# Kernel optimization log

Hardware: AMD Instinct MI355X
Metric: run time of the kernel (lower is better)

Reference implementation:

```python
import jax, jax.numpy as jnp
import numpy as np

N = 50000
E = 800000
F = 128
HID = 128
C = 40
GAMMA = 0.1
EPS = 0.1


def gcn(x, theta, src, dst, n):
    # GCNConv (bias=False) with added self-loops and symmetric normalization.
    xw = x @ theta  # [N, d]
    ones = jnp.ones(src.shape[0], dtype=x.dtype)
    deg = jax.ops.segment_sum(ones, dst, num_segments=n) + 1.0  # in-degree incl. self loop
    dinv = jax.lax.rsqrt(deg)
    norm = dinv[src] * dinv[dst]            # [E]
    msg = xw[src] * norm[:, None]           # [E, d]  (dominant memory traffic)
    agg = jax.ops.segment_sum(msg, dst, num_segments=n)
    return agg + xw * (dinv * dinv)[:, None]  # self-loop contribution


def antisym_conv(x, W, bias, theta, src, dst, n):
    # PyG AntiSymmetricConv, num_iters=1, act=tanh, eps=0.1, gamma=0.1
    M = W - W.T - GAMMA * jnp.eye(W.shape[0], dtype=x.dtype)
    h = gcn(x, theta, src, dst, n)
    h = x @ M.T + h + bias
    return x + EPS * jnp.tanh(h)


def setup_inputs() -> dict:
    key = jax.random.key(0)
    ks = jax.random.split(key, 12)
    s = 0.05
    return {
        "x": jax.random.normal(ks[0], (N, F), dtype=jnp.float32),
        "edge_index": jax.random.randint(ks[1], (2, E), 0, N, dtype=jnp.int64)
        if jax.config.jax_enable_x64 else jax.random.randint(ks[1], (2, E), 0, N, dtype=jnp.int32),
        # AntiSymmetricConv 1 (num_features channels)
        "W1": jax.random.normal(ks[2], (F, F), dtype=jnp.float32) * s,
        "b1": jnp.zeros((F,), dtype=jnp.float32),
        "T1": jax.random.normal(ks[3], (F, F), dtype=jnp.float32) * s,
        # AntiSymmetricConv 2 (nhid channels)
        "W2": jax.random.normal(ks[4], (HID, HID), dtype=jnp.float32) * s,
        "b2": jnp.zeros((HID,), dtype=jnp.float32),
        "T2": jax.random.normal(ks[5], (HID, HID), dtype=jnp.float32) * s,
        # Linear layers (torch convention: weight [out, in])
        "lw1": jax.random.normal(ks[6], (HID, F), dtype=jnp.float32) * s,
        "lb1": jnp.zeros((HID,), dtype=jnp.float32),
        "lw2": jax.random.normal(ks[7], (C, HID), dtype=jnp.float32) * s,
        "lb2": jnp.zeros((C,), dtype=jnp.float32),
    }


def reference(x, edge_index, W1, b1, T1, W2, b2, T2, lw1, lb1, lw2, lb2):
    src, dst = edge_index[0], edge_index[1]
    n = x.shape[0]
    # eval mode: dropout is identity
    h = antisym_conv(x, W1, b1, T1, src, dst, n)
    h = jax.nn.relu(h)
    h = h @ lw1.T + lb1
    h = jax.nn.relu(h)
    h = antisym_conv(h, W2, b2, T2, src, dst, n)
    h = jax.nn.relu(h)
    x1 = h
    logits = h @ lw2.T + lb2
    result = jax.nn.log_softmax(logits, axis=-1)
    return (result, x1)
```

## Files before the change

### kernel.cpp

```cpp
#include <hip/hip_runtime.h>
#include <hip/hip_bf16.h>
#include <math.h>

#define GAMMA_ 0.1f
#define EPS_ 0.1f
constexpr int BLK = 256;

typedef __attribute__((ext_vector_type(8))) short short8;
typedef __attribute__((ext_vector_type(4))) float f32x4;
typedef __attribute__((ext_vector_type(2))) float f32x2v;
typedef unsigned char u8;

__device__ inline float bflo(uint u) { union { uint i; float f; } v; v.i = u << 16; return v.f; }
__device__ inline float bfhi(uint u) { union { uint i; float f; } v; v.i = u & 0xffff0000u; return v.f; }
__device__ inline ushort f2bf(float f) {
  union { float f; uint i; } v; v.f = f;
  uint i = v.i;
  return (ushort)((i + 0x7fffu + ((i >> 16) & 1u)) >> 16);
}

#if __has_builtin(__builtin_amdgcn_cvt_pk_f32_fp8) && __has_builtin(__builtin_amdgcn_cvt_pk_fp8_f32)
#define HW_FP8 1
#endif

__device__ inline f32x2v fp8x2_dec(uint raw) {
#ifdef HW_FP8
  return __builtin_amdgcn_cvt_pk_f32_fp8(raw, false);
#else
  f32x2v r;
#pragma unroll
  for (int i = 0; i < 2; ++i) {
    uint b = (raw >> (8 * i)) & 0xffu;
    uint em = b & 0x7fu;
    union { uint u; float f; } o;
    o.u = ((b & 0x80u) << 24) | (0x3C000000u + (em << 20));
    r[i] = (em >= 8u) ? o.f : 0.f;
  }
  return r;
#endif
}

__device__ inline uint fp8enc1(float x) {
  union { float f; uint u; } v; v.f = x;
  uint s = (v.u >> 24) & 0x80u;
  uint a = v.u & 0x7fffffffu;
  if (a >= 0x43E00000u) return s | 0x7Eu;
  uint r = a + 0x7FFFFu + ((a >> 20) & 1u);
  if (r < 0x3D800000u) return s;
  return s | (((r - 0x3C000000u) >> 20) & 0x7fu);
}

template<bool HI>
__device__ inline uint fp8x2_enc(float f0, float f1, uint old) {
#ifdef HW_FP8
  return __builtin_amdgcn_cvt_pk_fp8_f32(f0, f1, old, HI);
#else
  uint p = fp8enc1(f0) | (fp8enc1(f1) << 8);
  return HI ? ((old & 0x0000ffffu) | (p << 16)) : ((old & 0xffff0000u) | p);
#endif
}

__global__ void k_init(int* cnt, int n) {
  int i = blockIdx.x * BLK + threadIdx.x;
  if (i < n) cnt[i] = 0;
}

__global__ void k_count(const int* __restrict__ dst, int* cnt,
                        int* __restrict__ rank, int e) {
  int i = blockIdx.x * BLK + threadIdx.x;
  if (i < e) rank[i] = atomicAdd(&cnt[dst[i]], 1);
}

__global__ void k_scan1(const int* __restrict__ cnt, int* __restrict__ rowp,
                        int* __restrict__ bsum, int n) {
  __shared__ int s[BLK];
  int t = threadIdx.x;
  int i = blockIdx.x * BLK + t;
  int v = (i < n) ? cnt[i] : 0;
  s[t] = v; __syncthreads();
  for (int off = 1; off < BLK; off <<= 1) {
    int u = (t >= off) ? s[t - off] : 0;
    __syncthreads();
    s[t] += u;
    __syncthreads();
  }
  if (i < n) rowp[i] = s[t] - v;
  if (t == BLK - 1) bsum[blockIdx.x] = s[t];
}

__global__ void k_scan2(const int* __restrict__ bsum, int* __restrict__ boff, int nb) {
  __shared__ int s[BLK];
  int t = threadIdx.x;
  int v = (t < nb) ? bsum[t] : 0;
  s[t] = v; __syncthreads();
  for (int off = 1; off < BLK; off <<= 1) {
    int u = (t >= off) ? s[t - off] : 0;
    __syncthreads();
    s[t] += u;
    __syncthreads();
  }
  if (t < nb) boff[t] = s[t] - v;
}

__global__ void k_scan3(const int* __restrict__ boff, int* __restrict__ rowp,
                        const int* __restrict__ cnt, float* __restrict__ dinv,
                        int n, int e) {
  int i = blockIdx.x * BLK + threadIdx.x;
  if (i < n) {
    rowp[i] += boff[blockIdx.x];
    dinv[i] = rsqrtf((float)cnt[i] + 1.0f);
    if (i == 0) rowp[n] = e;
  }
}

__global__ void k_fill(const int* __restrict__ src, const int* __restrict__ dst,
                       const int* __restrict__ rowp, const int* __restrict__ rank,
                       int* __restrict__ csrc, int e) {
  int i = blockIdx.x * BLK + threadIdx.x;
  if (i < e) {
    int d = dst[i];
    csrc[rowp[d] + rank[i]] = src[i];
  }
}

__global__ void k_pack(const float* __restrict__ W1, const float* __restrict__ T1,
                       const float* __restrict__ W2, const float* __restrict__ T2,
                       const float* __restrict__ lw1, const float* __restrict__ lw2,
                       ushort* __restrict__ Bpk1, ushort* __restrict__ Bpk2,
                       ushort* __restrict__ Bpkl, ushort* __restrict__ Bpk2l) {
  int idx = blockIdx.x * BLK + threadIdx.x;
  if (idx < 65536) {
    int which = idx >> 15;
    int e = idx & 32767;
    int k = e >> 8, c = e & 255;
    const float* W = which ? W2 : W1;
    const float* T = which ? T2 : T1;
    float v;
    if (c < 128) {
      v = T[k * 128 + c];
    } else {
      int cc = c - 128;
      v = W[cc * 128 + k] - W[k * 128 + cc] - ((cc == k) ? GAMMA_ : 0.f);
    }
    int kt = k >> 5, q = (k >> 3) & 3, j = k & 7;
    ushort* B = which ? Bpk2 : Bpk1;
    B[(((kt * 4 + q) * 256 + c) << 3) + j] = f2bf(v);
  } else if (idx < 81920) {
    int e = idx - 65536;
    int k = e >> 7, c = e & 127;
    float v = lw1[c * 128 + k];
    int kt = k >> 5, q = (k >> 3) & 3, j = k & 7;
    Bpkl[(((kt * 4 + q) * 128 + c) << 3) + j] = f2bf(v);
  } else {
    int e = idx - 81920;
    if (e < 6144) {
      int k = e / 48, c = e - k * 48;
      float v = (c < 40) ? lw2[c * 128 + k] : 0.f;
      int kt = k >> 5, q = (k >> 3) & 3, j = k & 7;
      Bpk2l[(((kt * 4 + q) * 48 + c) << 3) + j] = f2bf(v);
    }
  }
}

template<int NC, bool SPLIT, bool FP32A>
__global__ __launch_bounds__(256) void k_mgemm(
    const void* __restrict__ Av, int nrows,
    const ushort* __restrict__ Bpk, const float* __restrict__ bias,
    const float* __restrict__ dinv,
    ushort* __restrict__ O0, ushort* __restrict__ O1, u8* __restrict__ Oq) {
  constexpr int NCW = NC / 4;
  constexpr int NT = NCW / 16;
  __shared__ ushort Cs[32 * NC];
  const int t = threadIdx.x;
  const int w = t >> 6, l = t & 63;
  const int lr = l & 15, lq = l >> 4;
  const int r0 = blockIdx.x * 32;
  const int ar0 = min(r0 + lr, nrows - 1);
  const int ar1 = min(r0 + 16 + lr, nrows - 1);
  f32x4 acc[2][NT];
#pragma unroll
  for (int rf = 0; rf < 2; ++rf)
#pragma unroll
    for (int n = 0; n < NT; ++n) acc[rf][n] = f32x4{0.f, 0.f, 0.f, 0.f};
#pragma unroll
  for (int kt = 0; kt < 4; ++kt) {
    short8 af0, af1;
    if (FP32A) {
      const float* Ap0 = (const float*)Av + (size_t)ar0 * 128 + lq * 8 + kt * 32;
      const float* Ap1 = (const float*)Av + (size_t)ar1 * 128 + lq * 8 + kt * 32;
      float4 a0 = *(const float4*)(Ap0), a0b = *(const float4*)(Ap0 + 4);
      float4 a1 = *(const float4*)(Ap1), a1b = *(const float4*)(Ap1 + 4);
      af0[0] = (short)f2bf(a0.x); af0[1] = (short)f2bf(a0.y);
      af0[2] = (short)f2bf(a0.z); af0[3] = (short)f2bf(a0.w);
      af0[4] = (short)f2bf(a0b.x); af0[5] = (short)f2bf(a0b.y);
      af0[6] = (short)f2bf(a0b.z); af0[7] = (short)f2bf(a0b.w);
      af1[0] = (short)f2bf(a1.x); af1[1] = (short)f2bf(a1.y);
      af1[2] = (short)f2bf(a1.z); af1[3] = (short)f2bf(a1.w);
      af1[4] = (short)f2bf(a1b.x); af1[5] = (short)f2bf(a1b.y);
      af1[6] = (short)f2bf(a1b.z); af1[7] = (short)f2bf(a1b.w);
    } else {
      af0 = *(const short8*)((const ushort*)Av + (size_t)ar0 * 128 + lq * 8 + kt * 32);
      af1 = *(const short8*)((const ushort*)Av + (size_t)ar1 * 128 + lq * 8 + kt * 32);
    }
    const ushort* bbase = Bpk + ((size_t)((kt * 4 + lq) * NC) + w * NCW + lr) * 8;
#pragma unroll
    for (int n = 0; n < NT; ++n) {
      short8 bf = *(const short8*)(bbase + n * 16 * 8);
      acc[0][n] = __builtin_amdgcn_mfma_f32_16x16x32_bf16(af0, bf, acc[0][n], 0, 0, 0);
      acc[1][n] = __builtin_amdgcn_mfma_f32_16x16x32_bf16(af1, bf, acc[1][n], 0, 0, 0);
    }
  }
#pragma unroll
  for (int rf = 0; rf < 2; ++rf)
#pragma unroll
    for (int n = 0; n < NT; ++n)
#pragma unroll
      for (int r = 0; r < 4; ++r) {
        int row = rf * 16 + lq * 4 + r;
        int col = w * NCW + n * 16 + lr;
        float v = acc[rf][n][r];
        if (!SPLIT) v = fmaxf(v + bias[col], 0.f);
        int pcol = col ^ (((row >> 2) & 3) << 3);
        Cs[row * NC + pcol] = f2bf(v);
      }
  __syncthreads();
  if (SPLIT) {
#pragma unroll
    for (int it = 0; it < 2; ++it) {
      int idx = it * 256 + t;
      int row = idx >> 4, c8 = idx & 15;
      if (r0 + row < nrows) {
        int pc = (16 + (c8 ^ ((row >> 2) & 3))) * 8;
        uint4 v = *(const uint4*)(Cs + row * 256 + pc);
        *(uint4*)(O1 + (size_t)(r0 + row) * 128 + c8 * 8) = v;
      }
    }
#pragma unroll
    for (int it = 0; it < 2; ++it) {
      int idx = it * 256 + t;
      int row = idx >> 4, c8 = idx & 15;
      if (r0 + row < nrows) {
        float di = dinv[r0 + row];
        int pc = (c8 ^ ((row >> 2) & 3)) * 8;
        const uint* p = (const uint*)(Cs + row * 256 + pc);
        uint u0 = p[0], u1 = p[1], u2 = p[2], u3 = p[3];
        uint lo = fp8x2_enc<false>(bflo(u0) * di, bfhi(u0) * di, 0u);
        lo = fp8x2_enc<true>(bflo(u1) * di, bfhi(u1) * di, lo);
        uint hi = fp8x2_enc<false>(bflo(u2) * di, bfhi(u2) * di, 0u);
        hi = fp8x2_enc<true>(bflo(u3) * di, bfhi(u3) * di, hi);
        uint2 ov = { lo, hi };
        *(uint2*)(Oq + (size_t)(r0 + row) * 128 + c8 * 8) = ov;
      }
    }
  } else {
#pragma unroll
    for (int it = 0; it < 2; ++it) {
      int idx = it * 256 + t;
      int row = idx >> 4, c8 = idx & 15;
      if (r0 + row < nrows) {
        int pc = (c8 ^ ((row >> 2) & 3)) * 8;
        uint4 v = *(const uint4*)(Cs + row * 128 + pc);
        *(uint4*)(O0 + (size_t)(r0 + row) * 128 + c8 * 8) = v;
      }
    }
  }
}

template<bool XIN_BF, bool OUT_BF>
__global__ __launch_bounds__(256) void k_aggc(
    const u8* __restrict__ xq, const ushort* __restrict__ xmb,
    const float* __restrict__ xinf, const ushort* __restrict__ xinb,
    const float* __restrict__ dinv,
    const int* __restrict__ rowp, const int* __restrict__ csrc,
    const float* __restrict__ bias,
    float* __restrict__ outf, ushort* __restrict__ outb, int n) {
  int node = blockIdx.x * 4 + (threadIdx.x >> 6);
  if (node >= n) return;
  int l = threadIdx.x & 63;
  uint su = *(const ushort*)(xq + (size_t)node * 128 + 2 * l);
  f32x2v sf = fp8x2_dec(su);
  float a0 = sf[0], a1 = sf[1];
  int e0 = rowp[node], e1 = rowp[node + 1];
  int e = e0;
  for (; e + 7 < e1; e += 8) {
    int s[8];
#pragma unroll
    for (int u = 0; u < 8; ++u) s[u] = csrc[e + u];
    uint g[8];
#pragma unroll
    for (int u = 0; u < 8; ++u)
      g[u] = *(const ushort*)(xq + (size_t)s[u] * 128 + 2 * l);
#pragma unroll
    for (int u = 0; u < 8; ++u) {
      f32x2v f = fp8x2_dec(g[u]);
      a0 += f[0]; a1 += f[1];
    }
  }
  if (e + 3 < e1) {
    int s[4];
#pragma unroll
    for (int u = 0; u < 4; ++u) s[u] = csrc[e + u];
    uint g[4];
#pragma unroll
    for (int u = 0; u < 4; ++u)
      g[u] = *(const ushort*)(xq + (size_t)s[u] * 128 + 2 * l);
#pragma unroll
    for (int u = 0; u < 4; ++u) {
      f32x2v f = fp8x2_dec(g[u]);
      a0 += f[0]; a1 += f[1];
    }
    e += 4;
  }
  for (; e < e1; ++e) {
    uint g0 = *(const ushort*)(xq + (size_t)csrc[e] * 128 + 2 * l);
    f32x2v f = fp8x2_dec(g0);
    a0 += f[0]; a1 += f[1];
  }
  float di = dinv[node];
  uint mu = *(const uint*)(xmb + (size_t)node * 128 + 2 * l);
  float h0 = a0 * di + bflo(mu) + bias[2 * l];
  float h1 = a1 * di + bfhi(mu) + bias[2 * l + 1];
  float x0, x1v;
  if (XIN_BF) {
    uint xu = *(const uint*)(xinb + (size_t)node * 128 + 2 * l);
    x0 = bflo(xu); x1v = bfhi(xu);
  } else {
    float2 xv = *(const float2*)(xinf + (size_t)node * 128 + 2 * l);
    x0 = xv.x; x1v = xv.y;
  }
  float o0 = fmaxf(x0 + EPS_ * tanhf(h0), 0.f);
  float o1 = fmaxf(x1v + EPS_ * tanhf(h1), 0.f);
  if (OUT_BF) {
    ushort2 o = { f2bf(o0), f2bf(o1) };
    *(ushort2*)(outb + (size_t)node * 128 + 2 * l) = o;
  } else {
    float2 o = { o0, o1 };
    *(float2*)(outf + (size_t)node * 128 + 2 * l) = o;
  }
}

__global__ __launch_bounds__(256) void k_logits2(
    const float* __restrict__ X, const ushort* __restrict__ Bpk,
    const float* __restrict__ lb2, float* __restrict__ out, int n) {
  __shared__ float Ls[64 * 49];
  __shared__ float bl[48];
  const int t = threadIdx.x;
  if (t < 48) bl[t] = (t < 40) ? lb2[t] : 0.f;
  const int w = t >> 6, l = t & 63;
  const int lr = l & 15, lq = l >> 4;
  const int r0 = blockIdx.x * 64;
  const int ar = min(r0 + w * 16 + lr, n - 1);
  const float* Ap = X + (size_t)ar * 128 + lq * 8;
  f32x4 acc[3];
#pragma unroll
  for (int nn = 0; nn < 3; ++nn) acc[nn] = f32x4{0.f, 0.f, 0.f, 0.f};
#pragma unroll
  for (int kt = 0; kt < 4; ++kt) {
    float4 xa = *(const float4*)(Ap + kt * 32);
    float4 xc = *(const float4*)(Ap + kt * 32 + 4);
    short8 af;
    af[0] = (short)f2bf(xa.x); af[1] = (short)f2bf(xa.y);
    af[2] = (short)f2bf(xa.z); af[3] = (short)f2bf(xa.w);
    af[4] = (short)f2bf(xc.x); af[5] = (short)f2bf(xc.y);
    af[6] = (short)f2bf(xc.z); af[7] = (short)f2bf(xc.w);
    const ushort* bbase = Bpk + ((size_t)((kt * 4 + lq) * 48) + lr) * 8;
#pragma unroll
    for (int nn = 0; nn < 3; ++nn) {
      short8 bf = *(const short8*)(bbase + nn * 16 * 8);
      acc[nn] = __builtin_amdgcn_mfma_f32_16x16x32_bf16(af, bf, acc[nn], 0, 0, 0);
    }
  }
  __syncthreads();
#pragma unroll
  for (int nn = 0; nn < 3; ++nn)
#pragma unroll
    for (int r = 0; r < 4; ++r) {
      int row = w * 16 + lq * 4 + r;
      int col = nn * 16 + lr;
      Ls[row * 49 + col] = acc[nn][r] + bl[col];
    }
  __syncthreads();
  int row = t >> 2, q = t & 3;
  if (r0 + row >= n) return;
  const float* Lr = Ls + row * 49 + q * 10;
  float m = -1e30f;
#pragma unroll
  for (int c = 0; c < 10; ++c) m = fmaxf(m, Lr[c]);
  m = fmaxf(m, __shfl_xor(m, 1));
  m = fmaxf(m, __shfl_xor(m, 2));
  float s = 0.f;
#pragma unroll
  for (int c = 0; c < 10; ++c) s += expf(Lr[c] - m);
  s += __shfl_xor(s, 1);
  s += __shfl_xor(s, 2);
  float lse = m + logf(s);
  float* Or = out + (size_t)(r0 + row) * 40 + q * 10;
#pragma unroll
  for (int c = 0; c < 10; ++c) Or[c] = Lr[c] - lse;
}

extern "C" void kernel_launch(void* const* d_in, const int* in_sizes, int n_in,
                              void* d_out, int out_size, void* d_ws, size_t ws_size,
                              hipStream_t stream) {
  const float* x   = (const float*)d_in[0];
  const int*   ei  = (const int*)d_in[1];
  const float* W1  = (const float*)d_in[2];
  const float* b1  = (const float*)d_in[3];
  const float* T1  = (const float*)d_in[4];
  const float* W2  = (const float*)d_in[5];
  const float* b2  = (const float*)d_in[6];
  const float* T2  = (const float*)d_in[7];
  const float* lw1 = (const float*)d_in[8];
  const float* lb1 = (const float*)d_in[9];
  const float* lw2 = (const float*)d_in[10];
  const float* lb2 = (const float*)d_in[11];
  const int N = in_sizes[0] / 128;
  const int E = in_sizes[1] / 2;
  const int* src = ei;
  const int* dst = ei + E;

  float* ws = (float*)d_ws;
  size_t o = 0;
  float* dinv = ws;             o += N;
  int* cnt = (int*)(ws + o);    o += N;
  int* rowp = (int*)(ws + o);   o += (size_t)(N + 4);
  int* csrc = (int*)(ws + o);   o += E;
  int* rank = (int*)(ws + o);   o += E;
  int* bsum = (int*)(ws + o);   o += 256;
  int* boff = (int*)(ws + o);   o += 256;
  o = (o + 3) & ~(size_t)3;
  ushort* us = (ushort*)(ws + o);
  size_t uo = 0;
  ushort* Bpk1 = us + uo;       uo += 32768;
  ushort* Bpk2 = us + uo;       uo += 32768;
  ushort* Bpkl = us + uo;       uo += 16384;
  ushort* Bpk2l = us + uo;      uo += 6144;
  ushort* xmb  = us + uo;       uo += (size_t)N * 128;
  ushort* h1b  = us + uo;       uo += (size_t)N * 128;
  ushort* h2b  = us + uo;       uo += (size_t)N * 128;
  u8* xq = (u8*)(us + uo);

  float* outp = (float*)d_out;
  float* x1 = outp + (size_t)N * 40;

  int nb_n = (N + BLK - 1) / BLK;
  int nb_e = (E + BLK - 1) / BLK;
  int nb_r = (N + 31) / 32;

  k_init<<<nb_n, BLK, 0, stream>>>(cnt, N);
  k_count<<<nb_e, BLK, 0, stream>>>(dst, cnt, rank, E);
  k_scan1<<<nb_n, BLK, 0, stream>>>(cnt, rowp, bsum, N);
  k_scan2<<<1, BLK, 0, stream>>>(bsum, boff, nb_n);
  k_scan3<<<nb_n, BLK, 0, stream>>>(boff, rowp, cnt, dinv, N, E);
  k_fill<<<nb_e, BLK, 0, stream>>>(src, dst, rowp, rank, csrc, E);
  k_pack<<<344, BLK, 0, stream>>>(W1, T1, W2, T2, lw1, lw2, Bpk1, Bpk2, Bpkl, Bpk2l);

  k_mgemm<256, true, true><<<nb_r, 256, 0, stream>>>(
      x, N, Bpk1, nullptr, dinv, nullptr, xmb, xq);
  k_aggc<false, true><<<(N + 3) / 4, 256, 0, stream>>>(
      xq, xmb, x, nullptr, dinv, rowp, csrc, b1, nullptr, h1b, N);
  k_mgemm<128, false, false><<<nb_r, 256, 0, stream>>>(
      h1b, N, Bpkl, lb1, nullptr, h2b, nullptr, nullptr);
  k_mgemm<256, true, false><<<nb_r, 256, 0, stream>>>(
      h2b, N, Bpk2, nullptr, dinv, nullptr, xmb, xq);
  k_aggc<true, false><<<(N + 3) / 4, 256, 0, stream>>>(
      xq, xmb, nullptr, h2b, dinv, rowp, csrc, b2, x1, nullptr, N);
  k_logits2<<<(N + 63) / 64, 256, 0, stream>>>(x1, Bpk2l, lb2, outp, N);
}
```

Measured before the change: 192.8 us.

## Fuse first aggregation with lin1 GEMM and retile GEMM to 64-row LDS blocks

Adds a new kernel that performs the layer-1 neighbour aggregation for 32 nodes, stages the bf16 results in shared memory, and applies the lin1 MFMA GEMM with bias and ReLU in the same kernel. This removes the h1 intermediate buffer round-trip and one launch. The split GEMM now processes 64 rows per block with the A tile staged in swizzled LDS, so each B fragment is reused across four row tiles. The count-buffer init kernel is replaced by hipMemsetAsync. The fused kernel uses 512-thread blocks with serialized per-warp aggregation, which may reduce latency hiding on the gather.

```diff
diff --git a/kernel.cpp b/kernel.cpp
--- a/kernel.cpp
+++ b/kernel.cpp
@@ -58,11 +58,6 @@
   uint p = fp8enc1(f0) | (fp8enc1(f1) << 8);
   return HI ? ((old & 0x0000ffffu) | (p << 16)) : ((old & 0xffff0000u) | p);
 #endif
-}
-
-__global__ void k_init(int* cnt, int n) {
-  int i = blockIdx.x * BLK + threadIdx.x;
-  if (i < n) cnt[i] = 0;
 }
 
 __global__ void k_count(const int* __restrict__ dst, int* cnt,
@@ -162,118 +157,198 @@
   }
 }
 
-template<int NC, bool SPLIT, bool FP32A>
+template<bool FP32A>
 __global__ __launch_bounds__(256) void k_mgemm(
     const void* __restrict__ Av, int nrows,
-    const ushort* __restrict__ Bpk, const float* __restrict__ bias,
-    const float* __restrict__ dinv,
-    ushort* __restrict__ O0, ushort* __restrict__ O1, u8* __restrict__ Oq) {
-  constexpr int NCW = NC / 4;
-  constexpr int NT = NCW / 16;
-  __shared__ ushort Cs[32 * NC];
+    const ushort* __restrict__ Bpk, const float* __restrict__ dinv,
+    ushort* __restrict__ O1, u8* __restrict__ Oq) {
+  __shared__ ushort S[64 * 256];
+  const int t = threadIdx.x;
+  const int w = t >> 6, l = t & 63;
+  const int lr = l & 15, lq = l >> 4;
+  const int r0 = blockIdx.x * 64;
+#pragma unroll
+  for (int it = 0; it < 4; ++it) {
+    int chunk = it * 256 + t;
+    int row = chunk >> 4, c16 = chunk & 15;
+    int gr = min(r0 + row, nrows - 1);
+    ushort* p = S + row * 128 + (c16 ^ (row & 7)) * 8;
+    if (FP32A) {
+      const float* A = (const float*)Av + (size_t)gr * 128 + c16 * 8;
+      float4 v0 = *(const float4*)(A);
+      float4 v1 = *(const float4*)(A + 4);
+      ushort4 o0 = {f2bf(v0.x), f2bf(v0.y), f2bf(v0.z), f2bf(v0.w)};
+      ushort4 o1 = {f2bf(v1.x), f2bf(v1.y), f2bf(v1.z), f2bf(v1.w)};
+      *(ushort4*)(p) = o0;
+      *(ushort4*)(p + 4) = o1;
+    } else {
+      const ushort* A = (const ushort*)Av + (size_t)gr * 128 + c16 * 8;
+      *(uint4*)p = *(const uint4*)A;
+    }
+  }
+  __syncthreads();
+  f32x4 acc[4][4];
+#pragma unroll
+  for (int rt = 0; rt < 4; ++rt)
+#pragma unroll
+    for (int n = 0; n < 4; ++n) acc[rt][n] = f32x4{0.f, 0.f, 0.f, 0.f};
+#pragma unroll
+  for (int kt = 0; kt < 4; ++kt) {
+    short8 af[4];
+#pragma unroll
+    for (int rt = 0; rt < 4; ++rt) {
+      int row = rt * 16 + lr;
+      af[rt] = *(const short8*)(S + row * 128 + ((kt * 4 + lq) ^ (row & 7)) * 8);
+    }
+    const ushort* bbase = Bpk + ((size_t)((kt * 4 + lq) * 256) + w * 64 + lr) * 8;
+#pragma unroll
+    for (int n = 0; n < 4; ++n) {
+      short8 bf = *(const short8*)(bbase + n * 16 * 8);
+#pragma unroll
+      for (int rt = 0; rt < 4; ++rt)
+        acc[rt][n] = __builtin_amdgcn_mfma_f32_16x16x32_bf16(af[rt], bf, acc[rt][n], 0, 0, 0);
+    }
+  }
+  __syncthreads();
+#pragma unroll
+  for (int rt = 0; rt < 4; ++rt)
+#pragma unroll
+    for (int n = 0; n < 4; ++n)
+#pragma unroll
+      for (int r = 0; r < 4; ++r) {
+        int row = rt * 16 + lq * 4 + r;
+        int col = w * 64 + n * 16 + lr;
+        int pcol = col ^ (((row >> 2) & 3) << 3);
+        S[row * 256 + pcol] = f2bf(acc[rt][n][r]);
+      }
+  __syncthreads();
+#pragma unroll
+  for (int it = 0; it < 4; ++it) {
+    int idx = it * 256 + t;
+    int row = idx >> 4, c8 = idx & 15;
+    if (r0 + row < nrows) {
+      int pc = (16 + (c8 ^ ((row >> 2) & 3))) * 8;
+      uint4 v = *(const uint4*)(S + row * 256 + pc);
+      *(uint4*)(O1 + (size_t)(r0 + row) * 128 + c8 * 8) = v;
+    }
+  }
+#pragma unroll
+  for (int it = 0; it < 4; ++it) {
+    int idx = it * 256 + t;
+    int row = idx >> 4, c8 = idx & 15;
+    if (r0 + row < nrows) {
+      float di = dinv[r0 + row];
+      int pc = (c8 ^ ((row >> 2) & 3)) * 8;
+      const uint* p = (const uint*)(S + row * 256 + pc);
+      uint u0 = p[0], u1 = p[1], u2 = p[2], u3 = p[3];
+      uint lo = fp8x2_enc<false>(bflo(u0) * di, bfhi(u0) * di, 0u);
+      lo = fp8x2_enc<true>(bflo(u1) * di, bfhi(u1) * di, lo);
+      uint hi = fp8x2_enc<false>(bflo(u2) * di, bfhi(u2) * di, 0u);
+      hi = fp8x2_enc<true>(bflo(u3) * di, bfhi(u3) * di, hi);
+      uint2 ov = { lo, hi };
+      *(uint2*)(Oq + (size_t)(r0 + row) * 128 + c8 * 8) = ov;
+    }
+  }
+}
+
+__global__ __launch_bounds__(512) void k_aggl(
+    const u8* __restrict__ xq, const ushort* __restrict__ xmb,
+    const float* __restrict__ xinf, const float* __restrict__ dinv,
+    const int* __restrict__ rowp, const int* __restrict__ csrc,
+    const float* __restrict__ bias, const ushort* __restrict__ Bpkl,
+    const float* __restrict__ lb1, ushort* __restrict__ h2b, int n) {
+  __shared__ ushort Hs[32 * 128];
   const int t = threadIdx.x;
   const int w = t >> 6, l = t & 63;
   const int lr = l & 15, lq = l >> 4;
   const int r0 = blockIdx.x * 32;
-  const int ar0 = min(r0 + lr, nrows - 1);
-  const int ar1 = min(r0 + 16 + lr, nrows - 1);
-  f32x4 acc[2][NT];
-#pragma unroll
-  for (int rf = 0; rf < 2; ++rf)
-#pragma unroll
-    for (int n = 0; n < NT; ++n) acc[rf][n] = f32x4{0.f, 0.f, 0.f, 0.f};
+#pragma unroll
+  for (int i = 0; i < 4; ++i) {
+    int lrow = w * 4 + i;
+    int node = r0 + lrow;
+    float o0 = 0.f, o1 = 0.f;
+    if (node < n) {
+      uint su = *(const ushort*)(xq + (size_t)node * 128 + 2 * l);
+      f32x2v sf = fp8x2_dec(su);
+      float a0 = sf[0], a1 = sf[1];
+      int e0 = rowp[node], e1 = rowp[node + 1];
+      int e = e0;
+      for (; e + 7 < e1; e += 8) {
+        int s[8];
+#pragma unroll
+        for (int u = 0; u < 8; ++u) s[u] = csrc[e + u];
+        uint g[8];
+#pragma unroll
+        for (int u = 0; u < 8; ++u)
+          g[u] = *(const ushort*)(xq + (size_t)s[u] * 128 + 2 * l);
+#pragma unroll
+        for (int u = 0; u < 8; ++u) {
+          f32x2v f = fp8x2_dec(g[u]);
+          a0 += f[0]; a1 += f[1];
+        }
+      }
+      if (e + 3 < e1) {
+        int s[4];
+#pragma unroll
+        for (int u = 0; u < 4; ++u) s[u] = csrc[e + u];
+        uint g[4];
+#pragma unroll
+        for (int u = 0; u < 4; ++u)
+          g[u] = *(const ushort*)(xq + (size_t)s[u] * 128 + 2 * l);
+#pragma unroll
+        for (int u = 0; u < 4; ++u) {
+          f32x2v f = fp8x2_dec(g[u]);
+          a0 += f[0]; a1 += f[1];
+        }
+        e += 4;
+      }
+      for (; e < e1; ++e) {
+        uint g0 = *(const ushort*)(xq + (size_t)csrc[e] * 128 + 2 * l);
+        f32x2v f = fp8x2_dec(g0);
+        a0 += f[0]; a1 += f[1];
+      }
+      float di = dinv[node];
+      uint mu = *(const uint*)(xmb + (size_t)node * 128 + 2 * l);
+      float h0 = a0 * di + bflo(mu) + bias[2 * l];
+      float h1 = a1 * di + bfhi(mu) + bias[2 * l + 1];
+      float2 xv = *(const float2*)(xinf + (size_t)node * 128 + 2 * l);
+      o0 = fmaxf(xv.x + EPS_ * tanhf(h0), 0.f);
+      o1 = fmaxf(xv.y + EPS_ * tanhf(h1), 0.f);
+    }
+    ushort2 o = { f2bf(o0), f2bf(o1) };
+    *(ushort2*)(Hs + lrow * 128 + ((l >> 2) ^ (lrow & 7)) * 8 + (l & 3) * 2) = o;
+  }
+  __syncthreads();
+  f32x4 acc[2];
+  acc[0] = f32x4{0.f, 0.f, 0.f, 0.f};
+  acc[1] = f32x4{0.f, 0.f, 0.f, 0.f};
 #pragma unroll
   for (int kt = 0; kt < 4; ++kt) {
-    short8 af0, af1;
-    if (FP32A) {
-      const float* Ap0 = (const float*)Av + (size_t)ar0 * 128 + lq * 8 + kt * 32;
-      const float* Ap1 = (const float*)Av + (size_t)ar1 * 128 + lq * 8 + kt * 32;
-      float4 a0 = *(const float4*)(Ap0), a0b = *(const float4*)(Ap0 + 4);
-      float4 a1 = *(const float4*)(Ap1), a1b = *(const float4*)(Ap1 + 4);
-      af0[0] = (short)f2bf(a0.x); af0[1] = (short)f2bf(a0.y);
-      af0[2] = (short)f2bf(a0.z); af0[3] = (short)f2bf(a0.w);
-      af0[4] = (short)f2bf(a0b.x); af0[5] = (short)f2bf(a0b.y);
-      af0[6] = (short)f2bf(a0b.z); af0[7] = (short)f2bf(a0b.w);
-      af1[0] = (short)f2bf(a1.x); af1[1] = (short)f2bf(a1.y);
-      af1[2] = (short)f2bf(a1.z); af1[3] = (short)f2bf(a1.w);
-      af1[4] = (short)f2bf(a1b.x); af1[5] = (short)f2bf(a1b.y);
-      af1[6] = (short)f2bf(a1b.z); af1[7] = (short)f2bf(a1b.w);
-    } else {
-      af0 = *(const short8*)((const ushort*)Av + (size_t)ar0 * 128 + lq * 8 + kt * 32);
-      af1 = *(const short8*)((const ushort*)Av + (size_t)ar1 * 128 + lq * 8 + kt * 32);
-    }
-    const ushort* bbase = Bpk + ((size_t)((kt * 4 + lq) * NC) + w * NCW + lr) * 8;
-#pragma unroll
-    for (int n = 0; n < NT; ++n) {
-      short8 bf = *(const short8*)(bbase + n * 16 * 8);
-      acc[0][n] = __builtin_amdgcn_mfma_f32_16x16x32_bf16(af0, bf, acc[0][n], 0, 0, 0);
-      acc[1][n] = __builtin_amdgcn_mfma_f32_16x16x32_bf16(af1, bf, acc[1][n], 0, 0, 0);
-    }
-  }
-#pragma unroll
-  for (int rf = 0; rf < 2; ++rf)
-#pragma unroll
-    for (int n = 0; n < NT; ++n)
-#pragma unroll
-      for (int r = 0; r < 4; ++r) {
-        int row = rf * 16 + lq * 4 + r;
-        int col = w * NCW + n * 16 + lr;
-        float v = acc[rf][n][r];
-        if (!SPLIT) v = fmaxf(v + bias[col], 0.f);
-        int pcol = col ^ (((row >> 2) & 3) << 3);
-        Cs[row * NC + pcol] = f2bf(v);
-      }
-  __syncthreads();
-  if (SPLIT) {
-#pragma unroll
-    for (int it = 0; it < 2; ++it) {
-      int idx = it * 256 + t;
-      int row = idx >> 4, c8 = idx & 15;
-      if (r0 + row < nrows) {
-        int pc = (16 + (c8 ^ ((row >> 2) & 3))) * 8;
-        uint4 v = *(const uint4*)(Cs + row * 256 + pc);
-        *(uint4*)(O1 + (size_t)(r0 + row) * 128 + c8 * 8) = v;
-      }
-    }
-#pragma unroll
-    for (int it = 0; it < 2; ++it) {
-      int idx = it * 256 + t;
-      int row = idx >> 4, c8 = idx & 15;
-      if (r0 + row < nrows) {
-        float di = dinv[r0 + row];
-        int pc = (c8 ^ ((row >> 2) & 3)) * 8;
-        const uint* p = (const uint*)(Cs + row * 256 + pc);
-        uint u0 = p[0], u1 = p[1], u2 = p[2], u3 = p[3];
-        uint lo = fp8x2_enc<false>(bflo(u0) * di, bfhi(u0) * di, 0u);
-        lo = fp8x2_enc<true>(bflo(u1) * di, bfhi(u1) * di, lo);
-        uint hi = fp8x2_enc<false>(bflo(u2) * di, bfhi(u2) * di, 0u);
-        hi = fp8x2_enc<true>(bflo(u3) * di, bfhi(u3) * di, hi);
-        uint2 ov = { lo, hi };
-        *(uint2*)(Oq + (size_t)(r0 + row) * 128 + c8 * 8) = ov;
-      }
-    }
-  } else {
-#pragma unroll
-    for (int it = 0; it < 2; ++it) {
-      int idx = it * 256 + t;
-      int row = idx >> 4, c8 = idx & 15;
-      if (r0 + row < nrows) {
-        int pc = (c8 ^ ((row >> 2) & 3)) * 8;
-        uint4 v = *(const uint4*)(Cs + row * 128 + pc);
-        *(uint4*)(O0 + (size_t)(r0 + row) * 128 + c8 * 8) = v;
-      }
-    }
-  }
-}
-
-template<bool XIN_BF, bool OUT_BF>
+    short8 bf = *(const short8*)(Bpkl + ((size_t)((kt * 4 + lq) * 128) + w * 16 + lr) * 8);
+#pragma unroll
+    for (int rt = 0; rt < 2; ++rt) {
+      int row = rt * 16 + lr;
+      short8 af = *(const short8*)(Hs + row * 128 + ((kt * 4 + lq) ^ (row & 7)) * 8);
+      acc[rt] = __builtin_amdgcn_mfma_f32_16x16x32_bf16(af, bf, acc[rt], 0, 0, 0);
+    }
+  }
+  int col = w * 16 + lr;
+  float bv = lb1[col];
+#pragma unroll
+  for (int rt = 0; rt < 2; ++rt)
+#pragma unroll
+    for (int r = 0; r < 4; ++r) {
+      int row = rt * 16 + lq * 4 + r;
+      if (r0 + row < n)
+        h2b[(size_t)(r0 + row) * 128 + col] = f2bf(fmaxf(acc[rt][r] + bv, 0.f));
+    }
+}
+
 __global__ __launch_bounds__(256) void k_aggc(
     const u8* __restrict__ xq, const ushort* __restrict__ xmb,
-    const float* __restrict__ xinf, const ushort* __restrict__ xinb,
-    const float* __restrict__ dinv,
+    const ushort* __restrict__ xinb, const float* __restrict__ dinv,
     const int* __restrict__ rowp, const int* __restrict__ csrc,
-    const float* __restrict__ bias,
-    float* __restrict__ outf, ushort* __restrict__ outb, int n) {
+    const float* __restrict__ bias, float* __restrict__ outf, int n) {
   int node = blockIdx.x * 4 + (threadIdx.x >> 6);
   if (node >= n) return;
   int l = threadIdx.x & 63;
@@ -320,23 +395,11 @@
   uint mu = *(const uint*)(xmb + (size_t)node * 128 + 2 * l);
   float h0 = a0 * di + bflo(mu) + bias[2 * l];
   float h1 = a1 * di + bfhi(mu) + bias[2 * l + 1];
-  float x0, x1v;
-  if (XIN_BF) {
-    uint xu = *(const uint*)(xinb + (size_t)node * 128 + 2 * l);
-    x0 = bflo(xu); x1v = bfhi(xu);
-  } else {
-    float2 xv = *(const float2*)(xinf + (size_t)node * 128 + 2 * l);
-    x0 = xv.x; x1v = xv.y;
-  }
-  float o0 = fmaxf(x0 + EPS_ * tanhf(h0), 0.f);
-  float o1 = fmaxf(x1v + EPS_ * tanhf(h1), 0.f);
-  if (OUT_BF) {
-    ushort2 o = { f2bf(o0), f2bf(o1) };
-    *(ushort2*)(outb + (size_t)node * 128 + 2 * l) = o;
-  } else {
-    float2 o = { o0, o1 };
-    *(float2*)(outf + (size_t)node * 128 + 2 * l) = o;
-  }
+  uint xu = *(const uint*)(xinb + (size_t)node * 128 + 2 * l);
+  float o0 = fmaxf(bflo(xu) + EPS_ * tanhf(h0), 0.f);
+  float o1 = fmaxf(bfhi(xu) + EPS_ * tanhf(h1), 0.f);
+  float2 o = { o0, o1 };
+  *(float2*)(outf + (size_t)node * 128 + 2 * l) = o;
 }
 
 __global__ __launch_bounds__(256) void k_logits2(
@@ -436,7 +499,6 @@
   ushort* Bpkl = us + uo;       uo += 16384;
   ushort* Bpk2l = us + uo;      uo += 6144;
   ushort* xmb  = us + uo;       uo += (size_t)N * 128;
-  ushort* h1b  = us + uo;       uo += (size_t)N * 128;
   ushort* h2b  = us + uo;       uo += (size_t)N * 128;
   u8* xq = (u8*)(us + uo);
 
@@ -445,9 +507,9 @@
 
   int nb_n = (N + BLK - 1) / BLK;
   int nb_e = (E + BLK - 1) / BLK;
-  int nb_r = (N + 31) / 32;
-
-  k_init<<<nb_n, BLK, 0, stream>>>(cnt, N);
+  int nb_r = (N + 63) / 64;
+
+  hipMemsetAsync(cnt, 0, (size_t)N * sizeof(int), stream);
   k_count<<<nb_e, BLK, 0, stream>>>(dst, cnt, rank, E);
   k_scan1<<<nb_n, BLK, 0, stream>>>(cnt, rowp, bsum, N);
   k_scan2<<<1, BLK, 0, stream>>>(bsum, boff, nb_n);
@@ -455,15 +517,11 @@
   k_fill<<<nb_e, BLK, 0, stream>>>(src, dst, rowp, rank, csrc, E);
   k_pack<<<344, BLK, 0, stream>>>(W1, T1, W2, T2, lw1, lw2, Bpk1, Bpk2, Bpkl, Bpk2l);
 
-  k_mgemm<256, true, true><<<nb_r, 256, 0, stream>>>(
-      x, N, Bpk1, nullptr, dinv, nullptr, xmb, xq);
-  k_aggc<false, true><<<(N + 3) / 4, 256, 0, stream>>>(
-      xq, xmb, x, nullptr, dinv, rowp, csrc, b1, nullptr, h1b, N);
-  k_mgemm<128, false, false><<<nb_r, 256, 0, stream>>>(
-      h1b, N, Bpkl, lb1, nullptr, h2b, nullptr, nullptr);
-  k_mgemm<256, true, false><<<nb_r, 256, 0, stream>>>(
-      h2b, N, Bpk2, nullptr, dinv, nullptr, xmb, xq);
-  k_aggc<true, false><<<(N + 3) / 4, 256, 0, stream>>>(
-      xq, xmb, nullptr, h2b, dinv, rowp, csrc, b2, x1, nullptr, N);
+  k_mgemm<true><<<nb_r, 256, 0, stream>>>(x, N, Bpk1, dinv, xmb, xq);
+  k_aggl<<<(N + 31) / 32, 512, 0, stream>>>(
+      xq, xmb, x, dinv, rowp, csrc, b1, Bpkl, lb1, h2b, N);
+  k_mgemm<false><<<nb_r, 256, 0, stream>>>(h2b, N, Bpk2, dinv, xmb, xq);
+  k_aggc<<<(N + 3) / 4, 256, 0, stream>>>(
+      xq, xmb, h2b, dinv, rowp, csrc, b2, x1, N);
   k_logits2<<<(N + 63) / 64, 256, 0, stream>>>(x1, Bpk2l, lb2, outp, N);
 }
```

Result: faster. 185.6 us (-3.7%).
